# Performance work log

Measured on AMD Instinct MI355X. Metric: run time of the kernel, lower is better.

## Reference

```python
import math
import jax, jax.numpy as jnp
import numpy as np

NUM_BUCKETS = 32
MAX_DISTANCE = 128
B, T, E, H, D = 2, 2048, 1024, 16, 64
INIT_SCALE = 0.1


def _relative_position_bucket(rel, num_buckets=NUM_BUCKETS, max_distance=MAX_DISTANCE):
    # T5-style bucketing; rel is int [T, T]
    nb = num_buckets // 2
    buckets = (rel > 0).astype(jnp.int32) * nb
    rel_abs = jnp.abs(rel)
    max_exact = nb // 2
    is_small = rel_abs < max_exact
    # guard log(0); those positions are selected by is_small anyway
    val_large = max_exact + (
        jnp.log(jnp.maximum(rel_abs, 1).astype(jnp.float32) / max_exact)
        / math.log(max_distance / max_exact) * (nb - max_exact)
    ).astype(jnp.int32)
    val_large = jnp.minimum(val_large, nb - 1)
    return buckets + jnp.where(is_small, rel_abs, val_large)


def setup_inputs() -> dict:
    key = jax.random.key(0)
    ks = jax.random.split(key, 6)
    x = jax.random.normal(ks[0], (B, T, E), dtype=jnp.float32)
    # nn.Linear weights are [out_features, in_features], init normal(std=0.1)
    Wq = jax.random.normal(ks[1], (H * D, E), dtype=jnp.float32) * INIT_SCALE
    Wk = jax.random.normal(ks[2], (H * D, E), dtype=jnp.float32) * INIT_SCALE
    Wv = jax.random.normal(ks[3], (H * D, E), dtype=jnp.float32) * INIT_SCALE
    Wo = jax.random.normal(ks[4], (E, H * D), dtype=jnp.float32) * INIT_SCALE
    # nn.Embedding default init: standard normal
    rel_emb = jax.random.normal(ks[5], (NUM_BUCKETS, H), dtype=jnp.float32)
    return {"x": x, "Wq": Wq, "Wk": Wk, "Wv": Wv, "Wo": Wo, "rel_emb": rel_emb}


def reference(x, Wq, Wk, Wv, Wo, rel_emb):
    b, t, _ = x.shape
    scale = D ** (-0.5)
    q = jnp.einsum('bte,fe->btf', x, Wq).reshape(b, t, H, D).transpose(0, 2, 1, 3)
    k = jnp.einsum('bte,fe->btf', x, Wk).reshape(b, t, H, D).transpose(0, 2, 1, 3)
    v = jnp.einsum('bte,fe->btf', x, Wv).reshape(b, t, H, D).transpose(0, 2, 1, 3)
    attn = jnp.einsum('bhtd,bhsd->bhts', q, k) * scale  # [B,H,T,T]
    # T5 relative position bias
    pos = jnp.arange(t)
    rel = pos[:, None] - pos[None, :]
    buckets = _relative_position_bucket(rel)
    bias = rel_emb[buckets]                    # [T,T,H]
    attn = attn + bias.transpose(2, 0, 1)[None]  # [1,H,T,T]
    # causal mask (triu, diagonal=1)
    causal = jnp.triu(jnp.ones((t, t), dtype=bool), k=1)
    attn = jnp.where(causal[None, None], -jnp.inf, attn)
    attn = jax.nn.softmax(attn, axis=-1)
    out = jnp.einsum('bhts,bhsd->bhtd', attn, v).transpose(0, 2, 1, 3).reshape(b, t, H * D)
    return jnp.einsum('btf,ef->bte', out, Wo)
```

## Files before the change

kernel.cpp:

```cpp
#include <hip/hip_runtime.h>
#include <hip/hip_bf16.h>
#include <stdint.h>


typedef __attribute__((ext_vector_type(8))) short bf16x8;
typedef __attribute__((ext_vector_type(4))) float f32x4;

#define MFMA16(a, b, c) __builtin_amdgcn_mfma_f32_16x16x32_bf16((a), (b), (c), 0, 0, 0)

typedef __attribute__((address_space(1))) void gvoid_t;
typedef __attribute__((address_space(3))) void lvoid_t;

__device__ __forceinline__ void gload16(const void* g, void* l) {
    __builtin_amdgcn_global_load_lds((gvoid_t*)g, (lvoid_t*)l, 16, 0, 0);
}

__device__ __forceinline__ ushort f2bf_rne(float f) {
    union { float f; uint32_t u; } v; v.f = f;
    uint32_t u = v.u;
    return (ushort)((u + 0x7FFFu + ((u >> 16) & 1u)) >> 16);
}

__global__ void cvt_all(const float* __restrict__ x,
                        const float* __restrict__ wq, const float* __restrict__ wk,
                        const float* __restrict__ wv, const float* __restrict__ wo,
                        ushort* __restrict__ out) {
    int i = (blockIdx.x * 256 + threadIdx.x) * 4;
    int sel = i >> 20;
    const float* src; int off;
    if (sel < 4) { src = x; off = i; }
    else {
        src = (sel == 4) ? wq : (sel == 5) ? wk : (sel == 6) ? wv : wo;
        off = i & 1048575;
    }
    float4 f = *(const float4*)(src + off);
    ushort4 o;
    o.x = f2bf_rne(f.x); o.y = f2bf_rne(f.y);
    o.z = f2bf_rne(f.z); o.w = f2bf_rne(f.w);
    *(ushort4*)(out + i) = o;
}

__global__ void build_bias(const float* __restrict__ rel_emb, float* __restrict__ bias_tab) {
    int idx = blockIdx.x * 256 + threadIdx.x;
    int h = idx >> 11, rel = idx & 2047;
    int bucket;
    if (rel == 0) bucket = 0;
    else if (rel < 8) bucket = 16 + rel;
    else {
        int t;
        if      (rel >= 91) t = 7;
        else if (rel >= 64) t = 6;
        else if (rel >= 46) t = 5;
        else if (rel >= 32) t = 4;
        else if (rel >= 23) t = 3;
        else if (rel >= 16) t = 2;
        else if (rel >= 12) t = 1;
        else                t = 0;
        bucket = 24 + t;
    }
    bias_tab[idx] = rel_emb[bucket * 16 + h];
}

template<int MODE>
__global__ __launch_bounds__(256, MODE == 0 ? 3 : 4) void gemm_bt(
    const ushort* __restrict__ A,
    const ushort* __restrict__ W0, const ushort* __restrict__ W1, const ushort* __restrict__ W2,
    ushort* __restrict__ outq, ushort* __restrict__ outk, ushort* __restrict__ outvt,
    float* __restrict__ outf)
{
    constexpr int BM  = (MODE == 0) ? 128 : 64;
    constexpr int ACH = BM / 64;
    constexpr int MI  = (MODE == 0) ? 4 : 2;
    __shared__ __align__(16) ushort lsA[2][BM * 32];
    __shared__ __align__(16) ushort lsB[2][128 * 32];
    const int tid = threadIdx.x;
    const int lane = tid & 63, w = tid >> 6;
    const int g = lane >> 4, c16 = lane & 15;
    const int m0 = blockIdx.x * BM;
    const int wm = w >> 1, wn = w & 1;

    const ushort* W;
    int n0, widx = 0;
    if (MODE == 0) {
        widx = blockIdx.y >> 3;
        W = (widx == 0) ? W0 : (widx == 1) ? W1 : W2;
        n0 = (blockIdx.y & 7) * 128;
    } else {
        W = W0;
        n0 = blockIdx.y * 128;
    }

    f32x4 acc[MI][4];
    #pragma unroll
    for (int i = 0; i < MI; i++)
        #pragma unroll
        for (int j = 0; j < 4; j++) acc[i][j] = (f32x4){0.f, 0.f, 0.f, 0.f};

    int acrow[ACH], acj[ACH], bcrow[2], bcj[2];
    #pragma unroll
    for (int i = 0; i < ACH; i++) {
        int c = (i * 4 + w) * 64 + lane;
        acrow[i] = c >> 2; acj[i] = (c & 3) ^ ((acrow[i] >> 1) & 3);
    }
    #pragma unroll
    for (int i = 0; i < 2; i++) {
        int c = (i * 4 + w) * 64 + lane;
        bcrow[i] = c >> 2; bcj[i] = (c & 3) ^ ((bcrow[i] >> 1) & 3);
    }

    auto stage = [&](int buf, int kt) {
        #pragma unroll
        for (int i = 0; i < ACH; i++)
            gload16(A + (size_t)(m0 + acrow[i]) * 1024 + kt + acj[i] * 8,
                    &lsA[buf][(i * 4 + w) * 512]);
        #pragma unroll
        for (int i = 0; i < 2; i++)
            gload16(W + (size_t)(n0 + bcrow[i]) * 1024 + kt + bcj[i] * 8,
                    &lsB[buf][(i * 4 + w) * 512]);
    };

    stage(0, 0);
    __syncthreads();

    for (int it = 0; it < 32; ++it) {
        const int cur = it & 1;
        if (it < 31) stage(cur ^ 1, (it + 1) * 32);
        bf16x8 af[MI], bfv[4];
        #pragma unroll
        for (int mi = 0; mi < MI; mi++) {
            int row = wm * (16 * MI) + mi * 16 + c16;
            af[mi] = *(const bf16x8*)(&lsA[cur][row * 32 + ((g ^ ((row >> 1) & 3)) * 8)]);
        }
        #pragma unroll
        for (int ni = 0; ni < 4; ni++) {
            int row = wn * 64 + ni * 16 + c16;
            bfv[ni] = *(const bf16x8*)(&lsB[cur][row * 32 + ((g ^ ((row >> 1) & 3)) * 8)]);
        }
        #pragma unroll
        for (int mi = 0; mi < MI; mi++)
            #pragma unroll
            for (int ni = 0; ni < 4; ni++)
                acc[mi][ni] = MFMA16(af[mi], bfv[ni], acc[mi][ni]);
        __syncthreads();
    }

    #pragma unroll
    for (int mi = 0; mi < MI; mi++) {
        #pragma unroll
        for (int ni = 0; ni < 4; ni++) {
            int mg = m0 + wm * (16 * MI) + mi * 16 + g * 4;
            if (MODE == 0) {
                int f = n0 + wn * 64 + ni * 16 + c16;
                int h = f >> 6, d = f & 63;
                if (widx < 2) {
                    ushort* dst = (widx == 0) ? outq : outk;
                    #pragma unroll
                    for (int r = 0; r < 4; r++) {
                        int m = mg + r, b = m >> 11, t = m & 2047;
                        dst[((b * 16 + h) * 2048 + t) * 64 + d] = f2bf_rne(acc[mi][ni][r]);
                    }
                } else {
                    int b = mg >> 11, t = mg & 2047;
                    ushort4 pk;
                    pk.x = f2bf_rne(acc[mi][ni][0]); pk.y = f2bf_rne(acc[mi][ni][1]);
                    pk.z = f2bf_rne(acc[mi][ni][2]); pk.w = f2bf_rne(acc[mi][ni][3]);
                    *(ushort4*)(outvt + ((size_t)(b * 16 + h) * 64 + d) * 2048 + t) = pk;
                }
            } else {
                int ng = n0 + wn * 64 + ni * 16 + c16;
                #pragma unroll
                for (int r = 0; r < 4; r++) {
                    int m = mg + r;
                    outf[(size_t)m * 1024 + ng] = acc[mi][ni][r];
                }
            }
        }
    }
}

__global__ __launch_bounds__(256, 3) void attn_kernel(
    const ushort* __restrict__ qb_, const ushort* __restrict__ kb_,
    const ushort* __restrict__ vtb, const float* __restrict__ bias_tab,
    ushort* __restrict__ ob)
{
    __shared__ __align__(16) ushort KV[2][2][4096];
    __shared__ __align__(16) ushort Ps[4][16 * 72];

    const int tid = threadIdx.x, lane = tid & 63, w = tid >> 6;
    const int g = lane >> 4, c16 = lane & 15;
    const int bh = blockIdx.y;
    const int qb = (blockIdx.x + bh) & 31;
    const int b = bh >> 4, h = bh & 15;

    const ushort* qh = qb_ + (size_t)bh * 2048 * 64;
    const ushort* kh = kb_ + (size_t)bh * 2048 * 64;
    const ushort* vh = vtb + (size_t)bh * 64 * 2048;
    const float* bt = bias_tab + h * 2048;
    const int q0 = qb * 64;

    int crow[2], cj[2];
    #pragma unroll
    for (int i = 0; i < 2; i++) {
        int c = (i * 4 + w) * 64 + lane;
        crow[i] = c >> 3;
        cj[i] = (c & 7) ^ (crow[i] & 7);
    }

    auto stageKV = [&](int buf, int j64) {
        int k0 = j64 * 64;
        #pragma unroll
        for (int i = 0; i < 2; i++) {
            gload16(kh + (size_t)(k0 + crow[i]) * 64 + cj[i] * 8, &KV[buf][0][(i * 4 + w) * 512]);
            gload16(vh + (size_t)crow[i] * 2048 + k0 + cj[i] * 8, &KV[buf][1][(i * 4 + w) * 512]);
        }
    };

    const int qrow = q0 + w * 16 + c16;
    bf16x8 qf[2];
    #pragma unroll
    for (int kk = 0; kk < 2; kk++)
        qf[kk] = *(const bf16x8*)(qh + (size_t)qrow * 64 + kk * 32 + g * 8);

    stageKV(0, 0);
    __syncthreads();

    float m_run = -1e30f, l_run = 0.f;
    f32x4 o[4];
    #pragma unroll
    for (int ni = 0; ni < 4; ni++) o[ni] = (f32x4){0.f, 0.f, 0.f, 0.f};
    const float bias_far = bt[128];

    for (int j64 = 0; j64 <= qb; j64++) {
        const int cur = j64 & 1;
        if (j64 < qb) stageKV(cur ^ 1, j64 + 1);
        const ushort* Ks = KV[cur][0];
        const ushort* Vs = KV[cur][1];
        const int k0 = j64 * 64;

        f32x4 s[4];
        #pragma unroll
        for (int f = 0; f < 4; f++) s[f] = (f32x4){0.f, 0.f, 0.f, 0.f};
        __builtin_amdgcn_s_setprio(1);
        #pragma unroll
        for (int kk = 0; kk < 2; kk++) {
            #pragma unroll
            for (int f = 0; f < 4; f++) {
                int row = f * 16 + c16;
                bf16x8 a = *(const bf16x8*)(Ks + row * 64 + (((kk * 4 + g) ^ (row & 7)) * 8));
                s[f] = MFMA16(a, qf[kk], s[f]);
            }
        }
        __builtin_amdgcn_s_setprio(0);

        const bool near = (qb - j64) < 3;
        const bool diag = (j64 == qb);
        float p[4][4];
        float mt = -1e30f;
        #pragma unroll
        for (int f = 0; f < 4; f++) {
            #pragma unroll
            for (int r = 0; r < 4; r++) {
                int kpos = k0 + f * 16 + g * 4 + r;
                int rel = qrow - kpos;
                float lg;
                if (diag && rel < 0) lg = -1e30f;
                else {
                    float bias = near ? bt[rel] : bias_far;
                    lg = s[f][r] * 0.125f + bias;
                }
                p[f][r] = lg;
                mt = fmaxf(mt, lg);
            }
        }
        mt = fmaxf(mt, __shfl_xor(mt, 16));
        mt = fmaxf(mt, __shfl_xor(mt, 32));
        float m_new = fmaxf(m_run, mt);
        float alpha = __expf(m_run - m_new);
        float lt = 0.f;
        #pragma unroll
        for (int f = 0; f < 4; f++)
            #pragma unroll
            for (int r = 0; r < 4; r++) {
                float e = __expf(p[f][r] - m_new);
                p[f][r] = e;
                lt += e;
            }
        lt += __shfl_xor(lt, 16);
        lt += __shfl_xor(lt, 32);
        l_run = l_run * alpha + lt;
        m_run = m_new;
        #pragma unroll
        for (int ni = 0; ni < 4; ni++) {
            o[ni][0] *= alpha; o[ni][1] *= alpha; o[ni][2] *= alpha; o[ni][3] *= alpha;
        }

        #pragma unroll
        for (int f = 0; f < 4; f++) {
            ushort4 pk;
            pk.x = f2bf_rne(p[f][0]); pk.y = f2bf_rne(p[f][1]);
            pk.z = f2bf_rne(p[f][2]); pk.w = f2bf_rne(p[f][3]);
            *(ushort4*)(&Ps[w][c16 * 72 + f * 16 + g * 4]) = pk;
        }
        __builtin_amdgcn_s_setprio(1);
        #pragma unroll
        for (int kk = 0; kk < 2; kk++) {
            bf16x8 pf = *(const bf16x8*)(&Ps[w][c16 * 72 + kk * 32 + g * 8]);
            #pragma unroll
            for (int ni = 0; ni < 4; ni++) {
                int row = ni * 16 + c16;
                bf16x8 av = *(const bf16x8*)(Vs + row * 64 + (((kk * 4 + g) ^ (row & 7)) * 8));
                o[ni] = MFMA16(av, pf, o[ni]);
            }
        }
        __builtin_amdgcn_s_setprio(0);
        __syncthreads();
    }

    float inv = 1.f / l_run;
    size_t base = ((size_t)(b * 2048 + qrow)) * 1024 + h * 64;
    #pragma unroll
    for (int ni = 0; ni < 4; ni++) {
        ushort4 pk;
        pk.x = f2bf_rne(o[ni][0] * inv); pk.y = f2bf_rne(o[ni][1] * inv);
        pk.z = f2bf_rne(o[ni][2] * inv); pk.w = f2bf_rne(o[ni][3] * inv);
        *(ushort4*)(ob + base + ni * 16 + g * 4) = pk;
    }
}

extern "C" void kernel_launch(void* const* d_in, const int* in_sizes, int n_in,
                              void* d_out, int out_size, void* d_ws, size_t ws_size,
                              hipStream_t stream) {
    const float* x       = (const float*)d_in[0];
    const float* Wq      = (const float*)d_in[1];
    const float* Wk      = (const float*)d_in[2];
    const float* Wv      = (const float*)d_in[3];
    const float* Wo      = (const float*)d_in[4];
    const float* rel_emb = (const float*)d_in[5];

    char* ws = (char*)d_ws;
    ushort* xbf = (ushort*)(ws);
    ushort* wqb = (ushort*)(ws + (8u  << 20));
    ushort* wkb = (ushort*)(ws + (10u << 20));
    ushort* wvb = (ushort*)(ws + (12u << 20));
    ushort* wob = (ushort*)(ws + (14u << 20));
    ushort* qbf = (ushort*)(ws + (16u << 20));
    ushort* kbf = (ushort*)(ws + (24u << 20));
    ushort* vtb = (ushort*)(ws + (32u << 20));
    ushort* obf = (ushort*)(ws + (40u << 20));
    float*  btab = (float*)(ws + (48u << 20));

    cvt_all<<<8192, 256, 0, stream>>>(x, Wq, Wk, Wv, Wo, xbf);
    build_bias<<<128, 256, 0, stream>>>(rel_emb, btab);

    gemm_bt<0><<<dim3(32, 24), 256, 0, stream>>>(xbf, wqb, wkb, wvb, qbf, kbf, vtb, nullptr);
    attn_kernel<<<dim3(32, 32), 256, 0, stream>>>(qbf, kbf, vtb, btab, obf);
    gemm_bt<1><<<dim3(64, 8), 256, 0, stream>>>(obf, wob, nullptr, nullptr,
                                                nullptr, nullptr, nullptr, (float*)d_out);
}
```

Baseline: 210.7 us.

## Single-buffer KV tiles for occupancy, fold softmax scale into Q, specialize far-bias softmax

Drops the double-buffered K/V shared memory in favor of a single buffer loaded synchronously each iteration, halving LDS so launch bounds can target four blocks per CU. The 1/8 softmax scale is folded into the Q projection epilogue, and tiles far from the diagonal use a specialized softmax path that applies the constant far bias through the max instead of per element. The trade is lost overlap between global loads and compute, in exchange for higher occupancy and less per-element ALU work.

New measurement: 190.5 us. -9.6%, faster.

```diff
diff --git a/kernel.cpp b/kernel.cpp
--- a/kernel.cpp
+++ b/kernel.cpp
@@ -144,6 +144,7 @@
         __syncthreads();
     }
 
+    const float qs = (MODE == 0 && 0 == (blockIdx.y >> 3)) ? 0.125f : 1.0f;
     #pragma unroll
     for (int mi = 0; mi < MI; mi++) {
         #pragma unroll
@@ -157,7 +158,7 @@
                     #pragma unroll
                     for (int r = 0; r < 4; r++) {
                         int m = mg + r, b = m >> 11, t = m & 2047;
-                        dst[((b * 16 + h) * 2048 + t) * 64 + d] = f2bf_rne(acc[mi][ni][r]);
+                        dst[((b * 16 + h) * 2048 + t) * 64 + d] = f2bf_rne(acc[mi][ni][r] * qs);
                     }
                 } else {
                     int b = mg >> 11, t = mg & 2047;
@@ -178,12 +179,13 @@
     }
 }
 
-__global__ __launch_bounds__(256, 3) void attn_kernel(
+__global__ __launch_bounds__(256, 4) void attn_kernel(
     const ushort* __restrict__ qb_, const ushort* __restrict__ kb_,
     const ushort* __restrict__ vtb, const float* __restrict__ bias_tab,
     ushort* __restrict__ ob)
 {
-    __shared__ __align__(16) ushort KV[2][2][4096];
+    __shared__ __align__(16) ushort Ks[64 * 64];
+    __shared__ __align__(16) ushort Vs[64 * 64];
     __shared__ __align__(16) ushort Ps[4][16 * 72];
 
     const int tid = threadIdx.x, lane = tid & 63, w = tid >> 6;
@@ -206,24 +208,12 @@
         cj[i] = (c & 7) ^ (crow[i] & 7);
     }
 
-    auto stageKV = [&](int buf, int j64) {
-        int k0 = j64 * 64;
-        #pragma unroll
-        for (int i = 0; i < 2; i++) {
-            gload16(kh + (size_t)(k0 + crow[i]) * 64 + cj[i] * 8, &KV[buf][0][(i * 4 + w) * 512]);
-            gload16(vh + (size_t)crow[i] * 2048 + k0 + cj[i] * 8, &KV[buf][1][(i * 4 + w) * 512]);
-        }
-    };
-
     const int qrow = q0 + w * 16 + c16;
     bf16x8 qf[2];
     #pragma unroll
     for (int kk = 0; kk < 2; kk++)
         qf[kk] = *(const bf16x8*)(qh + (size_t)qrow * 64 + kk * 32 + g * 8);
 
-    stageKV(0, 0);
-    __syncthreads();
-
     float m_run = -1e30f, l_run = 0.f;
     f32x4 o[4];
     #pragma unroll
@@ -231,11 +221,14 @@
     const float bias_far = bt[128];
 
     for (int j64 = 0; j64 <= qb; j64++) {
-        const int cur = j64 & 1;
-        if (j64 < qb) stageKV(cur ^ 1, j64 + 1);
-        const ushort* Ks = KV[cur][0];
-        const ushort* Vs = KV[cur][1];
         const int k0 = j64 * 64;
+        __syncthreads();
+        #pragma unroll
+        for (int i = 0; i < 2; i++) {
+            gload16(kh + (size_t)(k0 + crow[i]) * 64 + cj[i] * 8, Ks + (i * 4 + w) * 512);
+            gload16(vh + (size_t)crow[i] * 2048 + k0 + cj[i] * 8, Vs + (i * 4 + w) * 512);
+        }
+        __syncthreads();
 
         f32x4 s[4];
         #pragma unroll
@@ -255,38 +248,54 @@
         const bool near = (qb - j64) < 3;
         const bool diag = (j64 == qb);
         float p[4][4];
-        float mt = -1e30f;
-        #pragma unroll
-        for (int f = 0; f < 4; f++) {
-            #pragma unroll
-            for (int r = 0; r < 4; r++) {
-                int kpos = k0 + f * 16 + g * 4 + r;
-                int rel = qrow - kpos;
-                float lg;
-                if (diag && rel < 0) lg = -1e30f;
-                else {
-                    float bias = near ? bt[rel] : bias_far;
-                    lg = s[f][r] * 0.125f + bias;
-                }
-                p[f][r] = lg;
-                mt = fmaxf(mt, lg);
-            }
-        }
-        mt = fmaxf(mt, __shfl_xor(mt, 16));
-        mt = fmaxf(mt, __shfl_xor(mt, 32));
-        float m_new = fmaxf(m_run, mt);
-        float alpha = __expf(m_run - m_new);
-        float lt = 0.f;
-        #pragma unroll
-        for (int f = 0; f < 4; f++)
-            #pragma unroll
-            for (int r = 0; r < 4; r++) {
-                float e = __expf(p[f][r] - m_new);
-                p[f][r] = e;
-                lt += e;
-            }
+        float m_new, lt = 0.f;
+        if (near) {
+            float mt = -1e30f;
+            #pragma unroll
+            for (int f = 0; f < 4; f++)
+                #pragma unroll
+                for (int r = 0; r < 4; r++) {
+                    int kpos = k0 + f * 16 + g * 4 + r;
+                    int rel = qrow - kpos;
+                    float lg;
+                    if (diag && rel < 0) lg = -1e30f;
+                    else lg = s[f][r] + bt[rel];
+                    p[f][r] = lg;
+                    mt = fmaxf(mt, lg);
+                }
+            mt = fmaxf(mt, __shfl_xor(mt, 16));
+            mt = fmaxf(mt, __shfl_xor(mt, 32));
+            m_new = fmaxf(m_run, mt);
+            #pragma unroll
+            for (int f = 0; f < 4; f++)
+                #pragma unroll
+                for (int r = 0; r < 4; r++) {
+                    float e = __expf(p[f][r] - m_new);
+                    p[f][r] = e;
+                    lt += e;
+                }
+        } else {
+            float mt = -1e30f;
+            #pragma unroll
+            for (int f = 0; f < 4; f++)
+                #pragma unroll
+                for (int r = 0; r < 4; r++) mt = fmaxf(mt, s[f][r]);
+            mt = fmaxf(mt, __shfl_xor(mt, 16));
+            mt = fmaxf(mt, __shfl_xor(mt, 32));
+            m_new = fmaxf(m_run, mt + bias_far);
+            float madj = m_new - bias_far;
+            #pragma unroll
+            for (int f = 0; f < 4; f++)
+                #pragma unroll
+                for (int r = 0; r < 4; r++) {
+                    float e = __expf(s[f][r] - madj);
+                    p[f][r] = e;
+                    lt += e;
+                }
+        }
         lt += __shfl_xor(lt, 16);
         lt += __shfl_xor(lt, 32);
+        float alpha = __expf(m_run - m_new);
         l_run = l_run * alpha + lt;
         m_run = m_new;
         #pragma unroll
@@ -313,7 +322,6 @@
             }
         }
         __builtin_amdgcn_s_setprio(0);
-        __syncthreads();
     }
 
     float inv = 1.f / l_run;
```
